# Kernel tuning notes

Hardware: AMD Instinct MI355X
Metric: run time of the kernel (lower is better)

Reference implementation:

```python
import jax, jax.numpy as jnp
import numpy as np

DN = ('NDHWC', 'DHWIO', 'NDHWC')
EPS = 1e-5  # torch BatchNorm default

def _conv(x, w, s):
    # Minkowski conv, kernel 3 centered: output coord j gathers input coords s*j + {-1,0,1}
    return jax.lax.conv_general_dilated(x, w, (s, s, s), ((1, 1),) * 3, dimension_numbers=DN)

def _convt(x, w):
    # stride-2 transpose conv, kernel 3 centered: output p gets input c where 2c in {p-1,p,p+1}
    return jax.lax.conv_general_dilated(x, w, (1, 1, 1), ((1, 2),) * 3,
                                        lhs_dilation=(2, 2, 2), dimension_numbers=DN)

def _down(m):
    # stride-2 coordinate map: a coarse voxel is active iff any of its 2x2x2 fine voxels is
    B, G = m.shape[0], m.shape[1]
    return m.reshape(B, G // 2, 2, G // 2, 2, G // 2, 2).any(axis=(2, 4, 6))

def _mbn(h, m, g, b):
    # MinkowskiBatchNorm: BatchNorm1d over the active (sparse) feature rows only
    mf = m[..., None].astype(h.dtype)
    h = h * mf
    cnt = jnp.maximum(jnp.sum(mf), 1.0)
    mean = jnp.sum(h, axis=(0, 1, 2, 3)) / cnt
    var = jnp.sum(((h - mean) * mf) ** 2, axis=(0, 1, 2, 3)) / cnt
    return ((h - mean) * jax.lax.rsqrt(var + EPS) * g + b) * mf


def setup_inputs() -> dict:
    key = jax.random.key(0)
    ks = jax.random.split(key, 8)
    B, G, Cin, Cout = 2, 64, 4, 16
    def w(k, shape, fan):
        return jax.random.normal(k, shape, jnp.float32) * np.float32(1.0 / np.sqrt(fan))
    return {
        'x': jax.random.normal(ks[0], (B, G, G, G, Cin), jnp.float32),
        'mask': jax.random.bernoulli(ks[1], 0.1, (B, G, G, G)),
        'w1': w(ks[2], (3, 3, 3, Cin, 8), 27 * Cin), 'g1': jnp.ones(8), 'b1': jnp.zeros(8),
        'w2': w(ks[3], (3, 3, 3, 8, 16), 27 * 8), 'g2': jnp.ones(16), 'b2': jnp.zeros(16),
        'w3': w(ks[4], (3, 3, 3, 16, 32), 27 * 16), 'g3': jnp.ones(32), 'b3': jnp.zeros(32),
        'w3t': w(ks[5], (3, 3, 3, 32, 16), 27 * 32), 'g3t': jnp.ones(16), 'b3t': jnp.zeros(16),
        'w2t': w(ks[6], (3, 3, 3, 32, 16), 27 * 32), 'g2t': jnp.ones(16), 'b2t': jnp.zeros(16),
        'w1x1': w(ks[7], (24, Cout), 24),
    }


def reference(x, mask, w1, g1, b1, w2, g2, b2, w3, g3, b3,
              w3t, g3t, b3t, w2t, g2t, b2t, w1x1):
    m1 = mask
    m2 = _down(m1)
    m4 = _down(m2)
    mf1 = m1[..., None].astype(x.dtype)

    xs = x * mf1                                      # sparse tensor: zero at inactive coords
    s1 = _mbn(_conv(xs, w1, 1), m1, g1, b1)           # block1, stride 1
    o = jax.nn.relu(s1)
    s2 = _mbn(_conv(o, w2, 2), m2, g2, b2)            # block2, stride 2
    o = jax.nn.relu(s2)
    s4 = _mbn(_conv(o, w3, 2), m4, g3, b3)            # block3, stride 4
    o = jax.nn.relu(s4)

    o = jax.nn.relu(_mbn(_convt(o, w3t), m2, g3t, b3t))   # block3_tr -> stride-2 coords
    o = jnp.concatenate([o, s2], axis=-1)                 # ME.cat(out, out_s2) -> 32 ch
    o = jax.nn.relu(_mbn(_convt(o, w2t), m1, g2t, b2t))   # block2_tr -> stride-1 coords
    o = jnp.concatenate([o, s1], axis=-1)                 # ME.cat(out, out_s1) -> 24 ch
    return jnp.einsum('bdhwc,co->bdhwo', o, w1x1) * mf1   # conv1_tr: 1x1x1 conv
```

## Files before the change

kernel.cpp:

```cpp
#include <hip/hip_runtime.h>

#define NVOX1 524288
#define NVOX2 65536
#define NVOX4 8192

#define ST_SUM1 16
#define ST_SQ1  24
#define ST_SUM2 32
#define ST_SQ2  48
#define ST_SUM3 64
#define ST_SQ3  96
#define ST_SUM3T 128
#define ST_SQ3T  144
#define ST_SUM2T 160
#define ST_SQ2T  176
#define FLAG_OFF 200
#define IC_N1 204
#define IC_N2 205
#define IC_N4 206
#define ST_ZERO 256

#define OFF_M1C 512
#define OFF_M2  (OFF_M1C + NVOX1)
#define OFF_M4  (OFF_M2 + NVOX2)
#define OFF_R1  (OFF_M4 + NVOX4)
#define OFF_R2  (OFF_R1 + NVOX1)
#define OFF_R4  (OFF_R2 + NVOX2)
#define OFF_L1  (OFF_R4 + NVOX4)
#define OFF_L2  (OFF_L1 + NVOX1)
#define OFF_L4  (OFF_L2 + NVOX2)
#define OFF_BC1 (OFF_L4 + NVOX4)
#define OFF_BC2 (OFF_BC1 + 2048)
#define OFF_BC4 (OFF_BC2 + 256)
#define OFF_NB1  (OFF_BC4 + 32)
#define OFF_NB2  (OFF_NB1 + NVOX1)
#define OFF_NB4  (OFF_NB2 + NVOX2)
#define OFF_NBT3 (OFF_NB4 + NVOX4)
#define OFF_NBT2 (OFF_NBT3 + NVOX2)
#define OFF_XC   (OFF_NBT2 + NVOX1)
#define OFF_H1C  (OFF_XC + NVOX1 * 4)
#define OFF_S2C  (OFF_H1C + NVOX1 * 8)
#define OFF_H3C  (OFF_S2C + NVOX2 * 16)
#define OFF_T3C  (OFF_H3C + NVOX4 * 32)

#define EPSBN 1e-5f

__device__ __forceinline__ void ttaps(int p, int gin, int* c, int* k, int* ok) {
  c[0] = p >> 1; k[0] = (p & 1) ? 0 : 1; ok[0] = 1;
  int cb = (p + 1) >> 1;
  int o = (p & 1) && (cb < gin);
  c[1] = o ? cb : 0; k[1] = 2; ok[1] = o;
}

__device__ __forceinline__ void stat_flush8(float* sum, float* sq, float* s_sum, float* s_sq, int t) {
#pragma unroll
  for (int off = 1; off < 64; off <<= 1)
#pragma unroll
    for (int c = 0; c < 8; c++) {
      sum[c] += __shfl_xor(sum[c], off, 64);
      sq[c]  += __shfl_xor(sq[c], off, 64);
    }
  if ((t & 63) == 0) {
#pragma unroll
    for (int c = 0; c < 8; c++) { atomicAdd(&s_sum[c], sum[c]); atomicAdd(&s_sq[c], sq[c]); }
  }
}

__global__ __launch_bounds__(256) void k_detect(const unsigned int* __restrict__ m,
                                                int* __restrict__ flags) {
  int tid = blockIdx.x * 256 + threadIdx.x;
  int hasf = 0, hasb = 0;
  for (int i = tid; i < NVOX1; i += 256 * 256) {
    unsigned int v = m[i];
    if (v == 0x3F800000u) hasf = 1;
    else if (v > 1u) hasb = 1;
  }
  hasf = __syncthreads_or(hasf);
  hasb = __syncthreads_or(hasb);
  if (threadIdx.x == 0) {
    if (hasf) atomicOr(&flags[0], 1);
    if (hasb) atomicOr(&flags[1], 1);
  }
}

__global__ __launch_bounds__(256) void k_canon(const void* __restrict__ mraw,
                                               int* __restrict__ m1c,
                                               const int* __restrict__ flags,
                                               int* __restrict__ blkcnt1) {
  int idx = blockIdx.x * 256 + threadIdx.x;
  int isf = flags[0], isb = flags[1];
  int v;
  if (isf)      v = (((const float*)mraw)[idx] != 0.f);
  else if (isb) v = (((const unsigned char*)mraw)[idx] != 0);
  else          v = (((const int*)mraw)[idx] != 0);
  m1c[idx] = v;
  int c = __syncthreads_count(v);
  if (threadIdx.x == 0) blkcnt1[blockIdx.x] = c;
}

__global__ __launch_bounds__(256) void k_down1(const int* __restrict__ m1,
                                               int* __restrict__ m2,
                                               int* __restrict__ blkcnt2) {
  int idx = blockIdx.x * 256 + threadIdx.x;
  int x = idx & 31, y = (idx >> 5) & 31, z = (idx >> 10) & 31, b = idx >> 15;
  int any = 0;
#pragma unroll
  for (int dz = 0; dz < 2; dz++)
#pragma unroll
    for (int dy = 0; dy < 2; dy++)
#pragma unroll
      for (int dx = 0; dx < 2; dx++)
        any |= m1[((b * 64 + 2 * z + dz) * 64 + 2 * y + dy) * 64 + 2 * x + dx];
  any = any ? 1 : 0;
  m2[idx] = any;
  int c = __syncthreads_count(any);
  if (threadIdx.x == 0) blkcnt2[blockIdx.x] = c;
}

__global__ __launch_bounds__(256) void k_down2(const int* __restrict__ m2,
                                               int* __restrict__ m4,
                                               int* __restrict__ blkcnt4) {
  int idx = blockIdx.x * 256 + threadIdx.x;
  int x = idx & 15, y = (idx >> 4) & 15, z = (idx >> 8) & 15, b = idx >> 12;
  int any = 0;
#pragma unroll
  for (int dz = 0; dz < 2; dz++)
#pragma unroll
    for (int dy = 0; dy < 2; dy++)
#pragma unroll
      for (int dx = 0; dx < 2; dx++)
        any |= m2[((b * 32 + 2 * z + dz) * 32 + 2 * y + dy) * 32 + 2 * x + dx];
  any = any ? 1 : 0;
  m4[idx] = any;
  int c = __syncthreads_count(any);
  if (threadIdx.x == 0) blkcnt4[blockIdx.x] = c;
}

__global__ __launch_bounds__(1024) void k_scan(int* __restrict__ bc1,
                                               int* __restrict__ bc2,
                                               int* __restrict__ bc4,
                                               int* __restrict__ cnts) {
  __shared__ int sA[2048], sB[2048];
  int* a; int n; int outIdx;
  if (blockIdx.x == 0)      { a = bc1; n = 2048; outIdx = IC_N1; }
  else if (blockIdx.x == 1) { a = bc2; n = 256;  outIdx = IC_N2; }
  else                      { a = bc4; n = 32;   outIdx = IC_N4; }
  int t = threadIdx.x;
  int i0 = t, i1 = t + 1024;
  int v0 = (i0 < n) ? a[i0] : 0;
  int v1 = (i1 < n) ? a[i1] : 0;
  sA[i0] = v0; sA[i1] = v1;
  __syncthreads();
  int* src = sA; int* dst = sB;
  for (int st = 1; st < 2048; st <<= 1) {
    int x0 = src[i0]; if (i0 >= st) x0 += src[i0 - st];
    int x1 = src[i1]; if (i1 >= st) x1 += src[i1 - st];
    dst[i0] = x0; dst[i1] = x1;
    __syncthreads();
    int* tmp = src; src = dst; dst = tmp;
  }
  if (i0 < n) a[i0] = src[i0] - v0;
  if (i1 < n) a[i1] = src[i1] - v1;
  if (t == 0) cnts[outIdx] = src[2047];
}

__global__ __launch_bounds__(256) void k_scatter(const int* __restrict__ m1,
                                                 const int* __restrict__ m2,
                                                 const int* __restrict__ m4,
                                                 const int* __restrict__ bc1,
                                                 const int* __restrict__ bc2,
                                                 const int* __restrict__ bc4,
                                                 int* __restrict__ list1,
                                                 int* __restrict__ list2,
                                                 int* __restrict__ list4,
                                                 int* __restrict__ rank1,
                                                 int* __restrict__ rank2,
                                                 int* __restrict__ rank4) {
  __shared__ int s_w[4];
  int bid = blockIdx.x, t = threadIdx.x;
  const int* mask; const int* base; int* list; int* rank; int lb;
  if (bid < 2048)      { mask = m1; base = bc1; list = list1; rank = rank1; lb = bid; }
  else if (bid < 2304) { mask = m2; base = bc2; list = list2; rank = rank2; lb = bid - 2048; }
  else                 { mask = m4; base = bc4; list = list4; rank = rank4; lb = bid - 2304; }
  int idx = lb * 256 + t;
  int act = mask[idx];
  unsigned long long b = __ballot(act != 0);
  int lane = t & 63, wid = t >> 6;
  if (lane == 0) s_w[wid] = __popcll(b);
  __syncthreads();
  int wbase = 0;
  for (int i = 0; i < wid; i++) wbase += s_w[i];
  if (act) {
    int pre = __popcll(b & ((1ull << lane) - 1ull));
    int pos = base[lb] + wbase + pre;
    list[pos] = idx;
    rank[idx] = pos;
  }
}

__global__ __launch_bounds__(256) void k_nbr(const int* __restrict__ m1,
                                             const int* __restrict__ m2,
                                             const int* __restrict__ m4,
                                             const int* __restrict__ list1,
                                             const int* __restrict__ list2,
                                             const int* __restrict__ list4,
                                             const int* __restrict__ cnts,
                                             int* __restrict__ nb1,
                                             int* __restrict__ nb2,
                                             int* __restrict__ nb4,
                                             int* __restrict__ nbt3,
                                             int* __restrict__ nbt2) {
  int mode = blockIdx.y;
  int tid = blockIdx.x * 256 + threadIdx.x;
  int stride = gridDim.x * 256;
  if (mode == 0) {
    int n = cnts[IC_N1];
    for (int i = tid; i < n; i += stride) {
      int v = list1[i];
      int vx = v & 63, vy = (v >> 6) & 63, vz = (v >> 12) & 63, vb = v >> 18;
      unsigned wbits = 0; int tap = 0;
#pragma unroll
      for (int kd = 0; kd < 3; kd++) { int d = vz + kd - 1; int okd = ((unsigned)d < 64u); int dc = okd ? d : 0;
#pragma unroll
        for (int kh = 0; kh < 3; kh++) { int h = vy + kh - 1; int okh = ((unsigned)h < 64u); int hc = okh ? h : 0;
#pragma unroll
          for (int kw = 0; kw < 3; kw++) { int ww = vx + kw - 1; int okw = ((unsigned)ww < 64u); int wc = okw ? ww : 0;
            int ni = ((vb * 64 + dc) * 64 + hc) * 64 + wc;
            int bit = (okd & okh & okw) & (m1[ni] != 0);
            wbits |= ((unsigned)bit) << tap; tap++;
          } } }
      nb1[i] = (int)wbits;
    }
  } else if (mode == 1) {
    int n = cnts[IC_N2];
    for (int i = tid; i < n; i += stride) {
      int v = list2[i];
      int vx = v & 31, vy = (v >> 5) & 31, vz = (v >> 10) & 31, vb = v >> 15;
      unsigned wbits = 0; int tap = 0;
#pragma unroll
      for (int kd = 0; kd < 3; kd++) { int d = 2 * vz + kd - 1; int okd = (d >= 0); int dc = okd ? d : 0;
#pragma unroll
        for (int kh = 0; kh < 3; kh++) { int h = 2 * vy + kh - 1; int okh = (h >= 0); int hc = okh ? h : 0;
#pragma unroll
          for (int kw = 0; kw < 3; kw++) { int ww = 2 * vx + kw - 1; int okw = (ww >= 0); int wc = okw ? ww : 0;
            int ni = ((vb * 64 + dc) * 64 + hc) * 64 + wc;
            int bit = (okd & okh & okw) & (m1[ni] != 0);
            wbits |= ((unsigned)bit) << tap; tap++;
          } } }
      nb2[i] = (int)wbits;
    }
  } else if (mode == 2) {
    int n = cnts[IC_N4];
    for (int i = tid; i < n; i += stride) {
      int v = list4[i];
      int vx = v & 15, vy = (v >> 4) & 15, vz = (v >> 8) & 15, vb = v >> 12;
      unsigned wbits = 0; int tap = 0;
#pragma unroll
      for (int kd = 0; kd < 3; kd++) { int d = 2 * vz + kd - 1; int okd = (d >= 0); int dc = okd ? d : 0;
#pragma unroll
        for (int kh = 0; kh < 3; kh++) { int h = 2 * vy + kh - 1; int okh = (h >= 0); int hc = okh ? h : 0;
#pragma unroll
          for (int kw = 0; kw < 3; kw++) { int ww = 2 * vx + kw - 1; int okw = (ww >= 0); int wc = okw ? ww : 0;
            int ni = ((vb * 32 + dc) * 32 + hc) * 32 + wc;
            int bit = (okd & okh & okw) & (m2[ni] != 0);
            wbits |= ((unsigned)bit) << tap; tap++;
          } } }
      nb4[i] = (int)wbits;
    }
  } else if (mode == 3) {
    int n = cnts[IC_N2];
    for (int i = tid; i < n; i += stride) {
      int v = list2[i];
      int px = v & 31, py = (v >> 5) & 31, pz = (v >> 10) & 31, vb = v >> 15;
      int czv[2], kzv[2], okz[2], cyv[2], kyv[2], oky[2], cxv[2], kxv[2], okx[2];
      ttaps(pz, 16, czv, kzv, okz);
      ttaps(py, 16, cyv, kyv, oky);
      ttaps(px, 16, cxv, kxv, okx);
      unsigned wbits = 0; int comb = 0;
#pragma unroll
      for (int dz = 0; dz < 2; dz++)
#pragma unroll
        for (int dy = 0; dy < 2; dy++)
#pragma unroll
          for (int dx = 0; dx < 2; dx++) {
            int ni = ((vb * 16 + czv[dz]) * 16 + cyv[dy]) * 16 + cxv[dx];
            int bit = (okz[dz] & oky[dy] & okx[dx]) & (m4[ni] != 0);
            wbits |= ((unsigned)bit) << comb; comb++;
          }
      nbt3[i] = (int)wbits;
    }
  } else {
    int n = cnts[IC_N1];
    for (int i = tid; i < n; i += stride) {
      int v = list1[i];
      int px = v & 63, py = (v >> 6) & 63, pz = (v >> 12) & 63, vb = v >> 18;
      int czv[2], kzv[2], okz[2], cyv[2], kyv[2], oky[2], cxv[2], kxv[2], okx[2];
      ttaps(pz, 32, czv, kzv, okz);
      ttaps(py, 32, cyv, kyv, oky);
      ttaps(px, 32, cxv, kxv, okx);
      unsigned wbits = 0; int comb = 0;
#pragma unroll
      for (int dz = 0; dz < 2; dz++)
#pragma unroll
        for (int dy = 0; dy < 2; dy++)
#pragma unroll
          for (int dx = 0; dx < 2; dx++) {
            int ni = ((vb * 32 + czv[dz]) * 32 + cyv[dy]) * 32 + cxv[dx];
            int bit = (okz[dz] & oky[dy] & okx[dx]) & (m2[ni] != 0);
            wbits |= ((unsigned)bit) << comb; comb++;
          }
      nbt2[i] = (int)wbits;
    }
  }
}

__global__ __launch_bounds__(256) void k_compact_x(const float* __restrict__ x,
                                                   const int* __restrict__ m1,
                                                   const int* __restrict__ rank1,
                                                   float* __restrict__ xc) {
  int v = blockIdx.x * 256 + threadIdx.x;
  if (!m1[v]) return;
  int r = rank1[v];
  float4 q = *(const float4*)(x + (size_t)v * 4);
  *(float4*)(xc + (size_t)r * 4) = q;
}

__global__ __launch_bounds__(256) void k_conv1(const float* __restrict__ xc,
                                               const int* __restrict__ rank1,
                                               const int* __restrict__ nb1,
                                               const int* __restrict__ list1,
                                               const int* __restrict__ cnts,
                                               const float* __restrict__ w,
                                               float* __restrict__ h1c,
                                               float* __restrict__ stats) {
  __shared__ float s_w[27 * 32];
  __shared__ float s_sum[8], s_sq[8];
  int t = threadIdx.x;
  { const float4* w4 = (const float4*)w; float4* sw4 = (float4*)s_w;
    for (int i = t; i < 216; i += 256) sw4[i] = w4[i]; }
  if (t < 8) { s_sum[t] = 0.f; s_sq[t] = 0.f; }
  __syncthreads();
  int n = cnts[IC_N1];
  float sum[8], sq[8];
#pragma unroll
  for (int c = 0; c < 8; c++) { sum[c] = 0.f; sq[c] = 0.f; }
  for (int i = blockIdx.x * 256 + t; i < n; i += gridDim.x * 256) {
    int v = list1[i];
    unsigned nbr = (unsigned)nb1[i];
    int vx = v & 63, vy = (v >> 6) & 63, vz = (v >> 12) & 63, vb = v >> 18;
    float acc[8];
#pragma unroll
    for (int c = 0; c < 8; c++) acc[c] = 0.f;
    int tap = 0;
#pragma unroll
    for (int kd = 0; kd < 3; kd++)
#pragma unroll
      for (int kh = 0; kh < 3; kh++)
#pragma unroll
        for (int kw = 0; kw < 3; kw++) {
          if (nbr & (1u << tap)) {
            int ni = ((vb * 64 + vz + kd - 1) * 64 + vy + kh - 1) * 64 + vx + kw - 1;
            int r = rank1[ni];
            float4 ip = *(const float4*)(xc + (size_t)r * 4);
            const float* wp = s_w + tap * 32;
#pragma unroll
            for (int co = 0; co < 8; co++) {
              float a = fmaf(ip.x, wp[co], acc[co]);
              a = fmaf(ip.y, wp[8 + co], a);
              a = fmaf(ip.z, wp[16 + co], a);
              acc[co] = fmaf(ip.w, wp[24 + co], a);
            }
          }
          tap++;
        }
    float4* hp = (float4*)(h1c + (size_t)i * 8);
    hp[0] = make_float4(acc[0], acc[1], acc[2], acc[3]);
    hp[1] = make_float4(acc[4], acc[5], acc[6], acc[7]);
#pragma unroll
    for (int c = 0; c < 8; c++) { sum[c] += acc[c]; sq[c] += acc[c] * acc[c]; }
  }
  stat_flush8(sum, sq, s_sum, s_sq, t);
  __syncthreads();
  if (t < 8) {
    if (s_sum[t] != 0.f) atomicAdd(&stats[ST_SUM1 + t], s_sum[t]);
    if (s_sq[t]  != 0.f) atomicAdd(&stats[ST_SQ1 + t], s_sq[t]);
  }
}

__global__ __launch_bounds__(256) void k_conv2(const float* __restrict__ h1c,
                                               const int* __restrict__ rank1,
                                               const int* __restrict__ nb2,
                                               const int* __restrict__ list2,
                                               const int* __restrict__ cnts,
                                               const float* __restrict__ w,
                                               const float* __restrict__ g1,
                                               const float* __restrict__ b1,
                                               float* __restrict__ s2c,
                                               float* __restrict__ stats) {
  __shared__ float s_w[27 * 8 * 8];
  __shared__ float s_sc[8], s_bi[8];
  __shared__ float s_sum[8], s_sq[8];
  int t = threadIdx.x, g = blockIdx.y;
  for (int i = t; i < 432; i += 256) {
    int r = i >> 1, half = i & 1;
    *(float4*)(s_w + r * 8 + half * 4) = *(const float4*)(w + r * 16 + g * 8 + half * 4);
  }
  if (t < 8) {
    float cnt = fmaxf((float)cnts[IC_N1], 1.f);
    float mean = stats[ST_SUM1 + t] / cnt;
    float var = fmaxf(stats[ST_SQ1 + t] / cnt - mean * mean, 0.f);
    float sc = g1[t] * rsqrtf(var + EPSBN);
    s_sc[t] = sc; s_bi[t] = b1[t] - mean * sc;
    s_sum[t] = 0.f; s_sq[t] = 0.f;
  }
  __syncthreads();
  int n = cnts[IC_N2];
  float sum[8], sq[8];
#pragma unroll
  for (int c = 0; c < 8; c++) { sum[c] = 0.f; sq[c] = 0.f; }
  for (int i = blockIdx.x * 256 + t; i < n; i += gridDim.x * 256) {
    int v = list2[i];
    unsigned nbr = (unsigned)nb2[i];
    int vx = v & 31, vy = (v >> 5) & 31, vz = (v >> 10) & 31, vb = v >> 15;
    float acc[8];
#pragma unroll
    for (int c = 0; c < 8; c++) acc[c] = 0.f;
    int tap = 0;
#pragma unroll
    for (int kd = 0; kd < 3; kd++)
#pragma unroll
      for (int kh = 0; kh < 3; kh++)
#pragma unroll
        for (int kw = 0; kw < 3; kw++) {
          if (nbr & (1u << tap)) {
            int ni = ((vb * 64 + 2 * vz + kd - 1) * 64 + 2 * vy + kh - 1) * 64 + 2 * vx + kw - 1;
            int r = rank1[ni];
            float4 i0 = *(const float4*)(h1c + (size_t)r * 8);
            float4 i1 = *(const float4*)(h1c + (size_t)r * 8 + 4);
            float rr[8] = {i0.x, i0.y, i0.z, i0.w, i1.x, i1.y, i1.z, i1.w};
            const float* wp = s_w + tap * 64;
#pragma unroll
            for (int ci = 0; ci < 8; ci++) {
              float vv = fmaxf(fmaf(rr[ci], s_sc[ci], s_bi[ci]), 0.f);
#pragma unroll
              for (int co = 0; co < 8; co++) acc[co] = fmaf(vv, wp[ci * 8 + co], acc[co]);
            }
          }
          tap++;
        }
    float4* sp = (float4*)(s2c + (size_t)i * 16 + g * 8);
    sp[0] = make_float4(acc[0], acc[1], acc[2], acc[3]);
    sp[1] = make_float4(acc[4], acc[5], acc[6], acc[7]);
#pragma unroll
    for (int c = 0; c < 8; c++) { sum[c] += acc[c]; sq[c] += acc[c] * acc[c]; }
  }
  stat_flush8(sum, sq, s_sum, s_sq, t);
  __syncthreads();
  if (t < 8) {
    if (s_sum[t] != 0.f) atomicAdd(&stats[ST_SUM2 + g * 8 + t], s_sum[t]);
    if (s_sq[t]  != 0.f) atomicAdd(&stats[ST_SQ2 + g * 8 + t], s_sq[t]);
  }
}

__global__ __launch_bounds__(256) void k_conv3(const float* __restrict__ s2c,
                                               const int* __restrict__ rank2,
                                               const int* __restrict__ nb4,
                                               const int* __restrict__ list4,
                                               const int* __restrict__ cnts,
                                               const float* __restrict__ w,
                                               const float* __restrict__ g2,
                                               const float* __restrict__ b2,
                                               float* __restrict__ h3c,
                                               float* __restrict__ stats) {
  __shared__ float s_w[27 * 16 * 8];
  __shared__ float s_sc[16], s_bi[16];
  __shared__ float s_sum[8], s_sq[8];
  int t = threadIdx.x, g = blockIdx.y;
  for (int i = t; i < 864; i += 256) {
    int r = i >> 1, half = i & 1;
    *(float4*)(s_w + r * 8 + half * 4) = *(const float4*)(w + r * 32 + g * 8 + half * 4);
  }
  if (t < 16) {
    float cnt = fmaxf((float)cnts[IC_N2], 1.f);
    float mean = stats[ST_SUM2 + t] / cnt;
    float var = fmaxf(stats[ST_SQ2 + t] / cnt - mean * mean, 0.f);
    float sc = g2[t] * rsqrtf(var + EPSBN);
    s_sc[t] = sc; s_bi[t] = b2[t] - mean * sc;
  }
  if (t < 8) { s_sum[t] = 0.f; s_sq[t] = 0.f; }
  __syncthreads();
  int n = cnts[IC_N4];
  float sum[8], sq[8];
#pragma unroll
  for (int c = 0; c < 8; c++) { sum[c] = 0.f; sq[c] = 0.f; }
  for (int i = blockIdx.x * 256 + t; i < n; i += gridDim.x * 256) {
    int v = list4[i];
    unsigned nbr = (unsigned)nb4[i];
    int vx = v & 15, vy = (v >> 4) & 15, vz = (v >> 8) & 15, vb = v >> 12;
    float acc[8];
#pragma unroll
    for (int c = 0; c < 8; c++) acc[c] = 0.f;
    int tap = 0;
#pragma unroll
    for (int kd = 0; kd < 3; kd++)
#pragma unroll
      for (int kh = 0; kh < 3; kh++)
#pragma unroll
        for (int kw = 0; kw < 3; kw++) {
          if (nbr & (1u << tap)) {
            int ni = ((vb * 32 + 2 * vz + kd - 1) * 32 + 2 * vy + kh - 1) * 32 + 2 * vx + kw - 1;
            int r = rank2[ni];
            const float4* ip = (const float4*)(s2c + (size_t)r * 16);
            const float* wp = s_w + tap * 128;
#pragma unroll
            for (int cq = 0; cq < 4; cq++) {
              float4 q = ip[cq];
              float rr[4] = {q.x, q.y, q.z, q.w};
#pragma unroll
              for (int j = 0; j < 4; j++) {
                int ci = cq * 4 + j;
                float vv = fmaxf(fmaf(rr[j], s_sc[ci], s_bi[ci]), 0.f);
#pragma unroll
                for (int co = 0; co < 8; co++) acc[co] = fmaf(vv, wp[ci * 8 + co], acc[co]);
              }
            }
          }
          tap++;
        }
    float4* hp = (float4*)(h3c + (size_t)i * 32 + g * 8);
    hp[0] = make_float4(acc[0], acc[1], acc[2], acc[3]);
    hp[1] = make_float4(acc[4], acc[5], acc[6], acc[7]);
#pragma unroll
    for (int c = 0; c < 8; c++) { sum[c] += acc[c]; sq[c] += acc[c] * acc[c]; }
  }
  stat_flush8(sum, sq, s_sum, s_sq, t);
  __syncthreads();
  if (t < 8) {
    if (s_sum[t] != 0.f) atomicAdd(&stats[ST_SUM3 + g * 8 + t], s_sum[t]);
    if (s_sq[t]  != 0.f) atomicAdd(&stats[ST_SQ3 + g * 8 + t], s_sq[t]);
  }
}

__global__ __launch_bounds__(256) void k_convt3(const float* __restrict__ h3c,
                                                const int* __restrict__ rank4,
                                                const int* __restrict__ nbt3,
                                                const int* __restrict__ list2,
                                                const int* __restrict__ cnts,
                                                const float* __restrict__ w,
                                                const float* __restrict__ g3,
                                                const float* __restrict__ b3,
                                                float* __restrict__ t3c,
                                                float* __restrict__ stats) {
  __shared__ float s_w[27 * 32 * 8];
  __shared__ float s_sc[32], s_bi[32];
  __shared__ float s_sum[8], s_sq[8];
  int t = threadIdx.x, g = blockIdx.y;
  for (int i = t; i < 1728; i += 256) {
    int r = i >> 1, half = i & 1;
    *(float4*)(s_w + r * 8 + half * 4) = *(const float4*)(w + r * 16 + g * 8 + half * 4);
  }
  if (t < 32) {
    float cnt = fmaxf((float)cnts[IC_N4], 1.f);
    float mean = stats[ST_SUM3 + t] / cnt;
    float var = fmaxf(stats[ST_SQ3 + t] / cnt - mean * mean, 0.f);
    float sc = g3[t] * rsqrtf(var + EPSBN);
    s_sc[t] = sc; s_bi[t] = b3[t] - mean * sc;
  }
  if (t < 8) { s_sum[t] = 0.f; s_sq[t] = 0.f; }
  __syncthreads();
  int n = cnts[IC_N2];
  float sum[8], sq[8];
#pragma unroll
  for (int c = 0; c < 8; c++) { sum[c] = 0.f; sq[c] = 0.f; }
  for (int i = blockIdx.x * 256 + t; i < n; i += gridDim.x * 256) {
    int v = list2[i];
    unsigned nbr = (unsigned)nbt3[i];
    int px = v & 31, py = (v >> 5) & 31, pz = (v >> 10) & 31, vb = v >> 15;
    int czv[2], kzv[2], okz[2], cyv[2], kyv[2], oky[2], cxv[2], kxv[2], okx[2];
    ttaps(pz, 16, czv, kzv, okz);
    ttaps(py, 16, cyv, kyv, oky);
    ttaps(px, 16, cxv, kxv, okx);
    float acc[8];
#pragma unroll
    for (int c = 0; c < 8; c++) acc[c] = 0.f;
    int comb = 0;
#pragma unroll
    for (int dz = 0; dz < 2; dz++)
#pragma unroll
      for (int dy = 0; dy < 2; dy++)
#pragma unroll
        for (int dx = 0; dx < 2; dx++) {
          if (nbr & (1u << comb)) {
            int ni = ((vb * 16 + czv[dz]) * 16 + cyv[dy]) * 16 + cxv[dx];
            int r = rank4[ni];
            const float4* ip = (const float4*)(h3c + (size_t)r * 32);
            const float* wp = s_w + ((kzv[dz] * 3 + kyv[dy]) * 3 + kxv[dx]) * 256;
#pragma unroll
            for (int cq = 0; cq < 8; cq++) {
              float4 q = ip[cq];
              float rr[4] = {q.x, q.y, q.z, q.w};
#pragma unroll
              for (int j = 0; j < 4; j++) {
                int ci = cq * 4 + j;
                float vv = fmaxf(fmaf(rr[j], s_sc[ci], s_bi[ci]), 0.f);
#pragma unroll
                for (int co = 0; co < 8; co++) acc[co] = fmaf(vv, wp[ci * 8 + co], acc[co]);
              }
            }
          }
          comb++;
        }
    float4* op = (float4*)(t3c + (size_t)i * 16 + g * 8);
    op[0] = make_float4(acc[0], acc[1], acc[2], acc[3]);
    op[1] = make_float4(acc[4], acc[5], acc[6], acc[7]);
#pragma unroll
    for (int c = 0; c < 8; c++) { sum[c] += acc[c]; sq[c] += acc[c] * acc[c]; }
  }
  stat_flush8(sum, sq, s_sum, s_sq, t);
  __syncthreads();
  if (t < 8) {
    if (s_sum[t] != 0.f) atomicAdd(&stats[ST_SUM3T + g * 8 + t], s_sum[t]);
    if (s_sq[t]  != 0.f) atomicAdd(&stats[ST_SQ3T + g * 8 + t], s_sq[t]);
  }
}

__global__ __launch_bounds__(256) void k_convt2(const float* __restrict__ t3c,
                                                const float* __restrict__ s2c,
                                                const int* __restrict__ rank2,
                                                const int* __restrict__ nbt2,
                                                const int* __restrict__ list1,
                                                const int* __restrict__ cnts,
                                                const float* __restrict__ w,
                                                const float* __restrict__ g3t,
                                                const float* __restrict__ b3t,
                                                const float* __restrict__ g2,
                                                const float* __restrict__ b2,
                                                float* __restrict__ outraw,
                                                float* __restrict__ stats) {
  __shared__ float s_w[27 * 32 * 8];
  __shared__ float s_sct[16], s_bit[16], s_sc2[16], s_bi2[16];
  __shared__ float s_sum[8], s_sq[8];
  int t = threadIdx.x, g = blockIdx.y;
  for (int i = t; i < 1728; i += 256) {
    int r = i >> 1, half = i & 1;
    *(float4*)(s_w + r * 8 + half * 4) = *(const float4*)(w + r * 16 + g * 8 + half * 4);
  }
  if (t < 16) {
    float cnt = fmaxf((float)cnts[IC_N2], 1.f);
    float mean = stats[ST_SUM3T + t] / cnt;
    float var = fmaxf(stats[ST_SQ3T + t] / cnt - mean * mean, 0.f);
    float sc = g3t[t] * rsqrtf(var + EPSBN);
    s_sct[t] = sc; s_bit[t] = b3t[t] - mean * sc;
    float mean2 = stats[ST_SUM2 + t] / cnt;
    float var2 = fmaxf(stats[ST_SQ2 + t] / cnt - mean2 * mean2, 0.f);
    float sc2 = g2[t] * rsqrtf(var2 + EPSBN);
    s_sc2[t] = sc2; s_bi2[t] = b2[t] - mean2 * sc2;
  }
  if (t < 8) { s_sum[t] = 0.f; s_sq[t] = 0.f; }
  __syncthreads();
  int n = cnts[IC_N1];
  float sum[8], sq[8];
#pragma unroll
  for (int c = 0; c < 8; c++) { sum[c] = 0.f; sq[c] = 0.f; }
  for (int i = blockIdx.x * 256 + t; i < n; i += gridDim.x * 256) {
    int v = list1[i];
    unsigned nbr = (unsigned)nbt2[i];
    int px = v & 63, py = (v >> 6) & 63, pz = (v >> 12) & 63, vb = v >> 18;
    int czv[2], kzv[2], okz[2], cyv[2], kyv[2], oky[2], cxv[2], kxv[2], okx[2];
    ttaps(pz, 32, czv, kzv, okz);
    ttaps(py, 32, cyv, kyv, oky);
    ttaps(px, 32, cxv, kxv, okx);
    float acc[8];
#pragma unroll
    for (int c = 0; c < 8; c++) acc[c] = 0.f;
    int comb = 0;
#pragma unroll
    for (int dz = 0; dz < 2; dz++)
#pragma unroll
      for (int dy = 0; dy < 2; dy++)
#pragma unroll
        for (int dx = 0; dx < 2; dx++) {
          if (nbr & (1u << comb)) {
            int ni = ((vb * 32 + czv[dz]) * 32 + cyv[dy]) * 32 + cxv[dx];
            int r = rank2[ni];
            const float4* tp = (const float4*)(t3c + (size_t)r * 16);
            const float4* sp = (const float4*)(s2c + (size_t)r * 16);
            const float* wp = s_w + ((kzv[dz] * 3 + kyv[dy]) * 3 + kxv[dx]) * 256;
#pragma unroll
            for (int cq = 0; cq < 4; cq++) {
              float4 q = tp[cq];
              float rr[4] = {q.x, q.y, q.z, q.w};
#pragma unroll
              for (int j = 0; j < 4; j++) {
                int ci = cq * 4 + j;
                float vv = fmaxf(fmaf(rr[j], s_sct[ci], s_bit[ci]), 0.f);
#pragma unroll
                for (int co = 0; co < 8; co++) acc[co] = fmaf(vv, wp[ci * 8 + co], acc[co]);
              }
            }
#pragma unroll
            for (int cq = 0; cq < 4; cq++) {
              float4 q = sp[cq];
              float rr[4] = {q.x, q.y, q.z, q.w};
#pragma unroll
              for (int j = 0; j < 4; j++) {
                int ci = cq * 4 + j;
                float vv = fmaf(rr[j], s_sc2[ci], s_bi2[ci]);
#pragma unroll
                for (int co = 0; co < 8; co++) acc[co] = fmaf(vv, wp[(16 + ci) * 8 + co], acc[co]);
              }
            }
          }
          comb++;
        }
    float4* op = (float4*)(outraw + (size_t)v * 16 + g * 8);
    op[0] = make_float4(acc[0], acc[1], acc[2], acc[3]);
    op[1] = make_float4(acc[4], acc[5], acc[6], acc[7]);
#pragma unroll
    for (int c = 0; c < 8; c++) { sum[c] += acc[c]; sq[c] += acc[c] * acc[c]; }
  }
  stat_flush8(sum, sq, s_sum, s_sq, t);
  __syncthreads();
  if (t < 8) {
    if (s_sum[t] != 0.f) atomicAdd(&stats[ST_SUM2T + g * 8 + t], s_sum[t]);
    if (s_sq[t]  != 0.f) atomicAdd(&stats[ST_SQ2T + g * 8 + t], s_sq[t]);
  }
}

__global__ __launch_bounds__(256) void k_final(float* __restrict__ out,
                                               const float* __restrict__ h1c,
                                               const int* __restrict__ m1,
                                               const int* __restrict__ rank1,
                                               const int* __restrict__ cnts,
                                               const float* __restrict__ g2t,
                                               const float* __restrict__ b2t,
                                               const float* __restrict__ g1,
                                               const float* __restrict__ b1,
                                               const float* __restrict__ w1x1,
                                               const float* __restrict__ stats) {
  __shared__ float s_sc[16], s_bi[16], s_sc1[8], s_bi1[8], s_w[384];
  int t = threadIdx.x;
  for (int i = t; i < 384; i += 256) s_w[i] = w1x1[i];
  if (t < 16) {
    float cnt = fmaxf((float)cnts[IC_N1], 1.f);
    float mean = stats[ST_SUM2T + t] / cnt;
    float var = fmaxf(stats[ST_SQ2T + t] / cnt - mean * mean, 0.f);
    float sc = g2t[t] * rsqrtf(var + EPSBN);
    s_sc[t] = sc; s_bi[t] = b2t[t] - mean * sc;
  }
  if (t < 8) {
    float cnt = fmaxf((float)cnts[IC_N1], 1.f);
    float mean = stats[ST_SUM1 + t] / cnt;
    float var = fmaxf(stats[ST_SQ1 + t] / cnt - mean * mean, 0.f);
    float sc = g1[t] * rsqrtf(var + EPSBN);
    s_sc1[t] = sc; s_bi1[t] = b1[t] - mean * sc;
  }
  __syncthreads();
  int v = blockIdx.x * 256 + t;
  float* op = out + (size_t)v * 16;
  float4* op4 = (float4*)op;
  if (!m1[v]) {
    float4 z = {0.f, 0.f, 0.f, 0.f};
    op4[0] = z; op4[1] = z; op4[2] = z; op4[3] = z;
    return;
  }
  int r = rank1[v];
  float t2[16];
  {
#pragma unroll
    for (int cq = 0; cq < 4; cq++) {
      float4 q = op4[cq];
      t2[cq * 4 + 0] = fmaxf(fmaf(q.x, s_sc[cq * 4 + 0], s_bi[cq * 4 + 0]), 0.f);
      t2[cq * 4 + 1] = fmaxf(fmaf(q.y, s_sc[cq * 4 + 1], s_bi[cq * 4 + 1]), 0.f);
      t2[cq * 4 + 2] = fmaxf(fmaf(q.z, s_sc[cq * 4 + 2], s_bi[cq * 4 + 2]), 0.f);
      t2[cq * 4 + 3] = fmaxf(fmaf(q.w, s_sc[cq * 4 + 3], s_bi[cq * 4 + 3]), 0.f);
    }
  }
  float s1v[8];
  {
    const float4* sp4 = (const float4*)(h1c + (size_t)r * 8);
#pragma unroll
    for (int cq = 0; cq < 2; cq++) {
      float4 q = sp4[cq];
      s1v[cq * 4 + 0] = fmaf(q.x, s_sc1[cq * 4 + 0], s_bi1[cq * 4 + 0]);
      s1v[cq * 4 + 1] = fmaf(q.y, s_sc1[cq * 4 + 1], s_bi1[cq * 4 + 1]);
      s1v[cq * 4 + 2] = fmaf(q.z, s_sc1[cq * 4 + 2], s_bi1[cq * 4 + 2]);
      s1v[cq * 4 + 3] = fmaf(q.w, s_sc1[cq * 4 + 3], s_bi1[cq * 4 + 3]);
    }
  }
  float o[16];
#pragma unroll
  for (int oc = 0; oc < 16; oc++) o[oc] = 0.f;
#pragma unroll
  for (int c = 0; c < 16; c++) {
    float vv = t2[c];
#pragma unroll
    for (int oc = 0; oc < 16; oc++) o[oc] = fmaf(vv, s_w[c * 16 + oc], o[oc]);
  }
#pragma unroll
  for (int c = 0; c < 8; c++) {
    float vv = s1v[c];
#pragma unroll
    for (int oc = 0; oc < 16; oc++) o[oc] = fmaf(vv, s_w[(16 + c) * 16 + oc], o[oc]);
  }
#pragma unroll
  for (int cq = 0; cq < 4; cq++) {
    float4 q = {o[cq * 4 + 0], o[cq * 4 + 1], o[cq * 4 + 2], o[cq * 4 + 3]};
    op4[cq] = q;
  }
}

extern "C" void kernel_launch(void* const* d_in, const int* in_sizes, int n_in,
                              void* d_out, int out_size, void* d_ws, size_t ws_size,
                              hipStream_t stream) {
  const float* x    = (const float*)d_in[0];
  const void*  mraw = d_in[1];
  const float* w1   = (const float*)d_in[2];
  const float* g1   = (const float*)d_in[3];
  const float* b1   = (const float*)d_in[4];
  const float* w2   = (const float*)d_in[5];
  const float* g2   = (const float*)d_in[6];
  const float* b2   = (const float*)d_in[7];
  const float* w3   = (const float*)d_in[8];
  const float* g3   = (const float*)d_in[9];
  const float* b3   = (const float*)d_in[10];
  const float* w3t  = (const float*)d_in[11];
  const float* g3t  = (const float*)d_in[12];
  const float* b3t  = (const float*)d_in[13];
  const float* w2t  = (const float*)d_in[14];
  const float* g2t  = (const float*)d_in[15];
  const float* b2t  = (const float*)d_in[16];
  const float* w1x1 = (const float*)d_in[17];

  float* ws = (float*)d_ws;
  float* stats = ws;
  int* cnts = (int*)ws;
  int* flags = (int*)(ws + FLAG_OFF);
  int* m1c = (int*)(ws + OFF_M1C);
  int* m2  = (int*)(ws + OFF_M2);
  int* m4  = (int*)(ws + OFF_M4);
  int* rank1 = (int*)(ws + OFF_R1);
  int* rank2 = (int*)(ws + OFF_R2);
  int* rank4 = (int*)(ws + OFF_R4);
  int* list1 = (int*)(ws + OFF_L1);
  int* list2 = (int*)(ws + OFF_L2);
  int* list4 = (int*)(ws + OFF_L4);
  int* bc1 = (int*)(ws + OFF_BC1);
  int* bc2 = (int*)(ws + OFF_BC2);
  int* bc4 = (int*)(ws + OFF_BC4);
  int* nb1  = (int*)(ws + OFF_NB1);
  int* nb2  = (int*)(ws + OFF_NB2);
  int* nb4  = (int*)(ws + OFF_NB4);
  int* nbt3 = (int*)(ws + OFF_NBT3);
  int* nbt2 = (int*)(ws + OFF_NBT2);
  float* xc  = ws + OFF_XC;
  float* h1c = ws + OFF_H1C;
  float* s2c = ws + OFF_S2C;
  float* h3c = ws + OFF_H3C;
  float* t3c = ws + OFF_T3C;
  float* out = (float*)d_out;

  hipMemsetAsync(ws, 0, ST_ZERO * sizeof(float), stream);
  k_detect<<<256, 256, 0, stream>>>((const unsigned int*)mraw, flags);
  k_canon<<<NVOX1 / 256, 256, 0, stream>>>(mraw, m1c, flags, bc1);
  k_down1<<<NVOX2 / 256, 256, 0, stream>>>(m1c, m2, bc2);
  k_down2<<<NVOX4 / 256, 256, 0, stream>>>(m2, m4, bc4);
  k_scan<<<3, 1024, 0, stream>>>(bc1, bc2, bc4, cnts);
  k_scatter<<<2048 + 256 + 32, 256, 0, stream>>>(m1c, m2, m4, bc1, bc2, bc4,
                                                 list1, list2, list4, rank1, rank2, rank4);
  k_nbr<<<dim3(256, 5), 256, 0, stream>>>(m1c, m2, m4, list1, list2, list4, cnts,
                                          nb1, nb2, nb4, nbt3, nbt2);
  k_compact_x<<<NVOX1 / 256, 256, 0, stream>>>(x, m1c, rank1, xc);
  k_conv1<<<256, 256, 0, stream>>>(xc, rank1, nb1, list1, cnts, w1, h1c, stats);
  k_conv2<<<dim3(256, 2), 256, 0, stream>>>(h1c, rank1, nb2, list2, cnts, w2, g1, b1, s2c, stats);
  k_conv3<<<dim3(32, 4), 256, 0, stream>>>(s2c, rank2, nb4, list4, cnts, w3, g2, b2, h3c, stats);
  k_convt3<<<dim3(256, 2), 256, 0, stream>>>(h3c, rank4, nbt3, list2, cnts, w3t, g3, b3, t3c, stats);
  k_convt2<<<dim3(256, 2), 256, 0, stream>>>(t3c, s2c, rank2, nbt2, list1, cnts, w2t,
                                             g3t, b3t, g2, b2, out, stats);
  k_final<<<NVOX1 / 256, 256, 0, stream>>>(out, h1c, m1c, rank1, cnts, g2t, b2t, g1, b1, w1x1, stats);
}
```

Measured before the change: 209.4 us.

## Split kernel taps across lanes in sparse convs with shuffle reduction

Each active voxel's sparse convolution taps are now spread over 4 lanes (conv1, conv2) or 2 lanes (the two transpose convs). Partial sums are combined with wavefront xor-shuffles, and only lane 0 writes the result and updates the statistics. Grid sizes grow to match. The aim is to hide gather latency and even out work from the irregular neighbour masks by giving the GPU more independent threads, at the cost of extra shuffles, redundant index decoding per lane, and idle lanes in the writeback.

```diff
diff --git a/kernel.cpp b/kernel.cpp
--- a/kernel.cpp
+++ b/kernel.cpp
@@ -340,44 +340,47 @@
     for (int i = t; i < 216; i += 256) sw4[i] = w4[i]; }
   if (t < 8) { s_sum[t] = 0.f; s_sq[t] = 0.f; }
   __syncthreads();
-  int n = cnts[IC_N1];
+  int n4 = cnts[IC_N1] * 4;
   float sum[8], sq[8];
 #pragma unroll
   for (int c = 0; c < 8; c++) { sum[c] = 0.f; sq[c] = 0.f; }
-  for (int i = blockIdx.x * 256 + t; i < n; i += gridDim.x * 256) {
+  for (int base = blockIdx.x * 256 + t; base < n4; base += gridDim.x * 256) {
+    int i = base >> 2, s = base & 3;
     int v = list1[i];
     unsigned nbr = (unsigned)nb1[i];
     int vx = v & 63, vy = (v >> 6) & 63, vz = (v >> 12) & 63, vb = v >> 18;
     float acc[8];
 #pragma unroll
     for (int c = 0; c < 8; c++) acc[c] = 0.f;
-    int tap = 0;
-#pragma unroll
-    for (int kd = 0; kd < 3; kd++)
-#pragma unroll
-      for (int kh = 0; kh < 3; kh++)
-#pragma unroll
-        for (int kw = 0; kw < 3; kw++) {
-          if (nbr & (1u << tap)) {
-            int ni = ((vb * 64 + vz + kd - 1) * 64 + vy + kh - 1) * 64 + vx + kw - 1;
-            int r = rank1[ni];
-            float4 ip = *(const float4*)(xc + (size_t)r * 4);
-            const float* wp = s_w + tap * 32;
-#pragma unroll
-            for (int co = 0; co < 8; co++) {
-              float a = fmaf(ip.x, wp[co], acc[co]);
-              a = fmaf(ip.y, wp[8 + co], a);
-              a = fmaf(ip.z, wp[16 + co], a);
-              acc[co] = fmaf(ip.w, wp[24 + co], a);
-            }
-          }
-          tap++;
+#pragma unroll 7
+    for (int k = s; k < 27; k += 4) {
+      if (nbr & (1u << k)) {
+        int kd = k / 9, krem = k - kd * 9, kh = krem / 3, kw = krem - kh * 3;
+        int ni = ((vb * 64 + vz + kd - 1) * 64 + vy + kh - 1) * 64 + vx + kw - 1;
+        int r = rank1[ni];
+        float4 ip = *(const float4*)(xc + (size_t)r * 4);
+        const float* wp = s_w + k * 32;
+#pragma unroll
+        for (int co = 0; co < 8; co++) {
+          float a = fmaf(ip.x, wp[co], acc[co]);
+          a = fmaf(ip.y, wp[8 + co], a);
+          a = fmaf(ip.z, wp[16 + co], a);
+          acc[co] = fmaf(ip.w, wp[24 + co], a);
         }
-    float4* hp = (float4*)(h1c + (size_t)i * 8);
-    hp[0] = make_float4(acc[0], acc[1], acc[2], acc[3]);
-    hp[1] = make_float4(acc[4], acc[5], acc[6], acc[7]);
-#pragma unroll
-    for (int c = 0; c < 8; c++) { sum[c] += acc[c]; sq[c] += acc[c] * acc[c]; }
+      }
+    }
+#pragma unroll
+    for (int c = 0; c < 8; c++) {
+      acc[c] += __shfl_xor(acc[c], 1, 64);
+      acc[c] += __shfl_xor(acc[c], 2, 64);
+    }
+    if (s == 0) {
+      float4* hp = (float4*)(h1c + (size_t)i * 8);
+      hp[0] = make_float4(acc[0], acc[1], acc[2], acc[3]);
+      hp[1] = make_float4(acc[4], acc[5], acc[6], acc[7]);
+#pragma unroll
+      for (int c = 0; c < 8; c++) { sum[c] += acc[c]; sq[c] += acc[c] * acc[c]; }
+    }
   }
   stat_flush8(sum, sq, s_sum, s_sq, t);
   __syncthreads();
@@ -414,45 +417,48 @@
     s_sum[t] = 0.f; s_sq[t] = 0.f;
   }
   __syncthreads();
-  int n = cnts[IC_N2];
+  int n4 = cnts[IC_N2] * 4;
   float sum[8], sq[8];
 #pragma unroll
   for (int c = 0; c < 8; c++) { sum[c] = 0.f; sq[c] = 0.f; }
-  for (int i = blockIdx.x * 256 + t; i < n; i += gridDim.x * 256) {
+  for (int base = blockIdx.x * 256 + t; base < n4; base += gridDim.x * 256) {
+    int i = base >> 2, s = base & 3;
     int v = list2[i];
     unsigned nbr = (unsigned)nb2[i];
     int vx = v & 31, vy = (v >> 5) & 31, vz = (v >> 10) & 31, vb = v >> 15;
     float acc[8];
 #pragma unroll
     for (int c = 0; c < 8; c++) acc[c] = 0.f;
-    int tap = 0;
-#pragma unroll
-    for (int kd = 0; kd < 3; kd++)
-#pragma unroll
-      for (int kh = 0; kh < 3; kh++)
-#pragma unroll
-        for (int kw = 0; kw < 3; kw++) {
-          if (nbr & (1u << tap)) {
-            int ni = ((vb * 64 + 2 * vz + kd - 1) * 64 + 2 * vy + kh - 1) * 64 + 2 * vx + kw - 1;
-            int r = rank1[ni];
-            float4 i0 = *(const float4*)(h1c + (size_t)r * 8);
-            float4 i1 = *(const float4*)(h1c + (size_t)r * 8 + 4);
-            float rr[8] = {i0.x, i0.y, i0.z, i0.w, i1.x, i1.y, i1.z, i1.w};
-            const float* wp = s_w + tap * 64;
-#pragma unroll
-            for (int ci = 0; ci < 8; ci++) {
-              float vv = fmaxf(fmaf(rr[ci], s_sc[ci], s_bi[ci]), 0.f);
-#pragma unroll
-              for (int co = 0; co < 8; co++) acc[co] = fmaf(vv, wp[ci * 8 + co], acc[co]);
-            }
-          }
-          tap++;
+#pragma unroll 7
+    for (int k = s; k < 27; k += 4) {
+      if (nbr & (1u << k)) {
+        int kd = k / 9, krem = k - kd * 9, kh = krem / 3, kw = krem - kh * 3;
+        int ni = ((vb * 64 + 2 * vz + kd - 1) * 64 + 2 * vy + kh - 1) * 64 + 2 * vx + kw - 1;
+        int r = rank1[ni];
+        float4 i0 = *(const float4*)(h1c + (size_t)r * 8);
+        float4 i1 = *(const float4*)(h1c + (size_t)r * 8 + 4);
+        float rr[8] = {i0.x, i0.y, i0.z, i0.w, i1.x, i1.y, i1.z, i1.w};
+        const float* wp = s_w + k * 64;
+#pragma unroll
+        for (int ci = 0; ci < 8; ci++) {
+          float vv = fmaxf(fmaf(rr[ci], s_sc[ci], s_bi[ci]), 0.f);
+#pragma unroll
+          for (int co = 0; co < 8; co++) acc[co] = fmaf(vv, wp[ci * 8 + co], acc[co]);
         }
-    float4* sp = (float4*)(s2c + (size_t)i * 16 + g * 8);
-    sp[0] = make_float4(acc[0], acc[1], acc[2], acc[3]);
-    sp[1] = make_float4(acc[4], acc[5], acc[6], acc[7]);
-#pragma unroll
-    for (int c = 0; c < 8; c++) { sum[c] += acc[c]; sq[c] += acc[c] * acc[c]; }
+      }
+    }
+#pragma unroll
+    for (int c = 0; c < 8; c++) {
+      acc[c] += __shfl_xor(acc[c], 1, 64);
+      acc[c] += __shfl_xor(acc[c], 2, 64);
+    }
+    if (s == 0) {
+      float4* sp = (float4*)(s2c + (size_t)i * 16 + g * 8);
+      sp[0] = make_float4(acc[0], acc[1], acc[2], acc[3]);
+      sp[1] = make_float4(acc[4], acc[5], acc[6], acc[7]);
+#pragma unroll
+      for (int c = 0; c < 8; c++) { sum[c] += acc[c]; sq[c] += acc[c] * acc[c]; }
+    }
   }
   stat_flush8(sum, sq, s_sum, s_sq, t);
   __syncthreads();
@@ -568,11 +574,12 @@
   }
   if (t < 8) { s_sum[t] = 0.f; s_sq[t] = 0.f; }
   __syncthreads();
-  int n = cnts[IC_N2];
+  int n2 = cnts[IC_N2] * 2;
   float sum[8], sq[8];
 #pragma unroll
   for (int c = 0; c < 8; c++) { sum[c] = 0.f; sq[c] = 0.f; }
-  for (int i = blockIdx.x * 256 + t; i < n; i += gridDim.x * 256) {
+  for (int base = blockIdx.x * 256 + t; base < n2; base += gridDim.x * 256) {
+    int i = base >> 1, s = base & 1;
     int v = list2[i];
     unsigned nbr = (unsigned)nbt3[i];
     int px = v & 31, py = (v >> 5) & 31, pz = (v >> 10) & 31, vb = v >> 15;
@@ -583,38 +590,37 @@
     float acc[8];
 #pragma unroll
     for (int c = 0; c < 8; c++) acc[c] = 0.f;
-    int comb = 0;
-#pragma unroll
-    for (int dz = 0; dz < 2; dz++)
-#pragma unroll
-      for (int dy = 0; dy < 2; dy++)
-#pragma unroll
-        for (int dx = 0; dx < 2; dx++) {
-          if (nbr & (1u << comb)) {
-            int ni = ((vb * 16 + czv[dz]) * 16 + cyv[dy]) * 16 + cxv[dx];
-            int r = rank4[ni];
-            const float4* ip = (const float4*)(h3c + (size_t)r * 32);
-            const float* wp = s_w + ((kzv[dz] * 3 + kyv[dy]) * 3 + kxv[dx]) * 256;
-#pragma unroll
-            for (int cq = 0; cq < 8; cq++) {
-              float4 q = ip[cq];
-              float rr[4] = {q.x, q.y, q.z, q.w};
-#pragma unroll
-              for (int j = 0; j < 4; j++) {
-                int ci = cq * 4 + j;
-                float vv = fmaxf(fmaf(rr[j], s_sc[ci], s_bi[ci]), 0.f);
-#pragma unroll
-                for (int co = 0; co < 8; co++) acc[co] = fmaf(vv, wp[ci * 8 + co], acc[co]);
-              }
-            }
+#pragma unroll 4
+    for (int k = s; k < 8; k += 2) {
+      if (nbr & (1u << k)) {
+        int dz = k >> 2, dy = (k >> 1) & 1, dx = k & 1;
+        int ni = ((vb * 16 + czv[dz]) * 16 + cyv[dy]) * 16 + cxv[dx];
+        int r = rank4[ni];
+        const float4* ip = (const float4*)(h3c + (size_t)r * 32);
+        const float* wp = s_w + ((kzv[dz] * 3 + kyv[dy]) * 3 + kxv[dx]) * 256;
+#pragma unroll
+        for (int cq = 0; cq < 8; cq++) {
+          float4 q = ip[cq];
+          float rr[4] = {q.x, q.y, q.z, q.w};
+#pragma unroll
+          for (int j = 0; j < 4; j++) {
+            int ci = cq * 4 + j;
+            float vv = fmaxf(fmaf(rr[j], s_sc[ci], s_bi[ci]), 0.f);
+#pragma unroll
+            for (int co = 0; co < 8; co++) acc[co] = fmaf(vv, wp[ci * 8 + co], acc[co]);
           }
-          comb++;
         }
-    float4* op = (float4*)(t3c + (size_t)i * 16 + g * 8);
-    op[0] = make_float4(acc[0], acc[1], acc[2], acc[3]);
-    op[1] = make_float4(acc[4], acc[5], acc[6], acc[7]);
-#pragma unroll
-    for (int c = 0; c < 8; c++) { sum[c] += acc[c]; sq[c] += acc[c] * acc[c]; }
+      }
+    }
+#pragma unroll
+    for (int c = 0; c < 8; c++) acc[c] += __shfl_xor(acc[c], 1, 64);
+    if (s == 0) {
+      float4* op = (float4*)(t3c + (size_t)i * 16 + g * 8);
+      op[0] = make_float4(acc[0], acc[1], acc[2], acc[3]);
+      op[1] = make_float4(acc[4], acc[5], acc[6], acc[7]);
+#pragma unroll
+      for (int c = 0; c < 8; c++) { sum[c] += acc[c]; sq[c] += acc[c] * acc[c]; }
+    }
   }
   stat_flush8(sum, sq, s_sum, s_sq, t);
   __syncthreads();
@@ -658,11 +664,12 @@
   }
   if (t < 8) { s_sum[t] = 0.f; s_sq[t] = 0.f; }
   __syncthreads();
-  int n = cnts[IC_N1];
+  int n2 = cnts[IC_N1] * 2;
   float sum[8], sq[8];
 #pragma unroll
   for (int c = 0; c < 8; c++) { sum[c] = 0.f; sq[c] = 0.f; }
-  for (int i = blockIdx.x * 256 + t; i < n; i += gridDim.x * 256) {
+  for (int base = blockIdx.x * 256 + t; base < n2; base += gridDim.x * 256) {
+    int i = base >> 1, s = base & 1;
     int v = list1[i];
     unsigned nbr = (unsigned)nbt2[i];
     int px = v & 63, py = (v >> 6) & 63, pz = (v >> 12) & 63, vb = v >> 18;
@@ -673,51 +680,50 @@
     float acc[8];
 #pragma unroll
     for (int c = 0; c < 8; c++) acc[c] = 0.f;
-    int comb = 0;
-#pragma unroll
-    for (int dz = 0; dz < 2; dz++)
-#pragma unroll
-      for (int dy = 0; dy < 2; dy++)
-#pragma unroll
-        for (int dx = 0; dx < 2; dx++) {
-          if (nbr & (1u << comb)) {
-            int ni = ((vb * 32 + czv[dz]) * 32 + cyv[dy]) * 32 + cxv[dx];
-            int r = rank2[ni];
-            const float4* tp = (const float4*)(t3c + (size_t)r * 16);
-            const float4* sp = (const float4*)(s2c + (size_t)r * 16);
-            const float* wp = s_w + ((kzv[dz] * 3 + kyv[dy]) * 3 + kxv[dx]) * 256;
-#pragma unroll
-            for (int cq = 0; cq < 4; cq++) {
-              float4 q = tp[cq];
-              float rr[4] = {q.x, q.y, q.z, q.w};
-#pragma unroll
-              for (int j = 0; j < 4; j++) {
-                int ci = cq * 4 + j;
-                float vv = fmaxf(fmaf(rr[j], s_sct[ci], s_bit[ci]), 0.f);
-#pragma unroll
-                for (int co = 0; co < 8; co++) acc[co] = fmaf(vv, wp[ci * 8 + co], acc[co]);
-              }
-            }
-#pragma unroll
-            for (int cq = 0; cq < 4; cq++) {
-              float4 q = sp[cq];
-              float rr[4] = {q.x, q.y, q.z, q.w};
-#pragma unroll
-              for (int j = 0; j < 4; j++) {
-                int ci = cq * 4 + j;
-                float vv = fmaf(rr[j], s_sc2[ci], s_bi2[ci]);
-#pragma unroll
-                for (int co = 0; co < 8; co++) acc[co] = fmaf(vv, wp[(16 + ci) * 8 + co], acc[co]);
-              }
-            }
+#pragma unroll 4
+    for (int k = s; k < 8; k += 2) {
+      if (nbr & (1u << k)) {
+        int dz = k >> 2, dy = (k >> 1) & 1, dx = k & 1;
+        int ni = ((vb * 32 + czv[dz]) * 32 + cyv[dy]) * 32 + cxv[dx];
+        int r = rank2[ni];
+        const float4* tp = (const float4*)(t3c + (size_t)r * 16);
+        const float4* sp = (const float4*)(s2c + (size_t)r * 16);
+        const float* wp = s_w + ((kzv[dz] * 3 + kyv[dy]) * 3 + kxv[dx]) * 256;
+#pragma unroll
+        for (int cq = 0; cq < 4; cq++) {
+          float4 q = tp[cq];
+          float rr[4] = {q.x, q.y, q.z, q.w};
+#pragma unroll
+          for (int j = 0; j < 4; j++) {
+            int ci = cq * 4 + j;
+            float vv = fmaxf(fmaf(rr[j], s_sct[ci], s_bit[ci]), 0.f);
+#pragma unroll
+            for (int co = 0; co < 8; co++) acc[co] = fmaf(vv, wp[ci * 8 + co], acc[co]);
           }
-          comb++;
         }
-    float4* op = (float4*)(outraw + (size_t)v * 16 + g * 8);
-    op[0] = make_float4(acc[0], acc[1], acc[2], acc[3]);
-    op[1] = make_float4(acc[4], acc[5], acc[6], acc[7]);
-#pragma unroll
-    for (int c = 0; c < 8; c++) { sum[c] += acc[c]; sq[c] += acc[c] * acc[c]; }
+#pragma unroll
+        for (int cq = 0; cq < 4; cq++) {
+          float4 q = sp[cq];
+          float rr[4] = {q.x, q.y, q.z, q.w};
+#pragma unroll
+          for (int j = 0; j < 4; j++) {
+            int ci = cq * 4 + j;
+            float vv = fmaf(rr[j], s_sc2[ci], s_bi2[ci]);
+#pragma unroll
+            for (int co = 0; co < 8; co++) acc[co] = fmaf(vv, wp[(16 + ci) * 8 + co], acc[co]);
+          }
+        }
+      }
+    }
+#pragma unroll
+    for (int c = 0; c < 8; c++) acc[c] += __shfl_xor(acc[c], 1, 64);
+    if (s == 0) {
+      float4* op = (float4*)(outraw + (size_t)v * 16 + g * 8);
+      op[0] = make_float4(acc[0], acc[1], acc[2], acc[3]);
+      op[1] = make_float4(acc[4], acc[5], acc[6], acc[7]);
+#pragma unroll
+      for (int c = 0; c < 8; c++) { sum[c] += acc[c]; sq[c] += acc[c] * acc[c]; }
+    }
   }
   stat_flush8(sum, sq, s_sum, s_sq, t);
   __syncthreads();
@@ -871,11 +877,11 @@
   k_nbr<<<dim3(256, 5), 256, 0, stream>>>(m1c, m2, m4, list1, list2, list4, cnts,
                                           nb1, nb2, nb4, nbt3, nbt2);
   k_compact_x<<<NVOX1 / 256, 256, 0, stream>>>(x, m1c, rank1, xc);
-  k_conv1<<<256, 256, 0, stream>>>(xc, rank1, nb1, list1, cnts, w1, h1c, stats);
-  k_conv2<<<dim3(256, 2), 256, 0, stream>>>(h1c, rank1, nb2, list2, cnts, w2, g1, b1, s2c, stats);
+  k_conv1<<<1024, 256, 0, stream>>>(xc, rank1, nb1, list1, cnts, w1, h1c, stats);
+  k_conv2<<<dim3(512, 2), 256, 0, stream>>>(h1c, rank1, nb2, list2, cnts, w2, g1, b1, s2c, stats);
   k_conv3<<<dim3(32, 4), 256, 0, stream>>>(s2c, rank2, nb4, list4, cnts, w3, g2, b2, h3c, stats);
-  k_convt3<<<dim3(256, 2), 256, 0, stream>>>(h3c, rank4, nbt3, list2, cnts, w3t, g3, b3, t3c, stats);
-  k_convt2<<<dim3(256, 2), 256, 0, stream>>>(t3c, s2c, rank2, nbt2, list1, cnts, w2t,
-                                             g3t, b3t, g2, b2, out, stats);
+  k_convt3<<<dim3(512, 2), 256, 0, stream>>>(h3c, rank4, nbt3, list2, cnts, w3t, g3, b3, t3c, stats);
+  k_convt2<<<dim3(1024, 2), 256, 0, stream>>>(t3c, s2c, rank2, nbt2, list1, cnts, w2t,
+                                              g3t, b3t, g2, b2, out, stats);
   k_final<<<NVOX1 / 256, 256, 0, stream>>>(out, h1c, m1c, rank1, cnts, g2t, b2t, g1, b1, w1x1, stats);
 }
```

New measurement: 216.2 us. +3.3%, slower.
